# Kernel optimization log

Hardware: AMD Instinct MI355X
Metric: run time of the kernel (lower is better)

## Reference

```python
import jax, jax.numpy as jnp
import numpy as np

D_MODEL = 1024
N_HEADS = 16
DFF = 4096
B, S = 2, 2048
EPS = 1e-6


def _dense_params(key, d_in, d_out):
    kw, kb = jax.random.split(key)
    w = jax.random.normal(kw, (d_in, d_out), jnp.float32) * 0.02
    b = jax.random.normal(kb, (d_out,), jnp.float32) * 0.02
    return w, b


def setup_inputs() -> dict:
    key = jax.random.key(0)
    ks = jax.random.split(key, 20)
    inp = {
        "x": jax.random.normal(ks[0], (B, S, D_MODEL), jnp.float32),
        "enc_output": jax.random.normal(ks[1], (B, S, D_MODEL), jnp.float32),
        # causal look-ahead mask: 1 where attention is NOT allowed
        "look_ahead_mask": jnp.triu(jnp.ones((S, S), jnp.float32), k=1)[None, None],
        "padding_mask": (jax.random.uniform(ks[2], (B, 1, 1, S)) < 0.1).astype(jnp.float32),
    }
    names = ["mha1_wq", "mha1_wk", "mha1_wv", "mha1_wo",
             "mha2_wq", "mha2_wk", "mha2_wv", "mha2_wo"]
    for i, n in enumerate(names):
        w, b = _dense_params(ks[3 + i], D_MODEL, D_MODEL)
        inp[n] = w
        inp[n.replace("w", "b")] = b
    inp["ffn_w1"], inp["ffn_b1"] = _dense_params(ks[11], D_MODEL, DFF)
    inp["ffn_w2"], inp["ffn_b2"] = _dense_params(ks[12], DFF, D_MODEL)
    for i, n in enumerate(["ln1", "ln2", "ln3"]):
        inp[n + "_g"] = jnp.ones((D_MODEL,), jnp.float32)
        inp[n + "_b"] = jnp.zeros((D_MODEL,), jnp.float32)
    return inp


def _layernorm(x, g, b):
    mu = jnp.mean(x, axis=-1, keepdims=True)
    var = jnp.mean(jnp.square(x - mu), axis=-1, keepdims=True)
    return (x - mu) * jax.lax.rsqrt(var + EPS) * g + b


def _mha(v, k, q, mask, wq, bq, wk, bk, wv, bv, wo, bo):
    Bq, Sq, D = q.shape
    depth = D // N_HEADS

    def split(t):  # [B,S,D] -> [B,H,S,depth]
        return t.reshape(t.shape[0], -1, N_HEADS, depth).transpose(0, 2, 1, 3)

    qh = split(q @ wq + bq)
    kh = split(k @ wk + bk)
    vh = split(v @ wv + bv)
    logits = jnp.einsum("bhqd,bhkd->bhqk", qh, kh) / jnp.sqrt(jnp.float32(depth))
    if mask is not None:
        logits = logits + mask * (-1e9)
    attn = jax.nn.softmax(logits, axis=-1)
    out = jnp.einsum("bhqk,bhkd->bhqd", attn, vh)
    out = out.transpose(0, 2, 1, 3).reshape(Bq, Sq, D)
    return out @ wo + bo


def reference(x, enc_output, look_ahead_mask, padding_mask,
              mha1_wq, mha1_bq, mha1_wk, mha1_bk, mha1_wv, mha1_bv, mha1_wo, mha1_bo,
              mha2_wq, mha2_bq, mha2_wk, mha2_bk, mha2_wv, mha2_bv, mha2_wo, mha2_bo,
              ffn_w1, ffn_b1, ffn_w2, ffn_b2,
              ln1_g, ln1_b, ln2_g, ln2_b, ln3_g, ln3_b):
    # self-attention (training=False -> dropout is identity)
    attn1 = _mha(x, x, x, look_ahead_mask,
                 mha1_wq, mha1_bq, mha1_wk, mha1_bk, mha1_wv, mha1_bv, mha1_wo, mha1_bo)
    out1 = _layernorm(x + attn1, ln1_g, ln1_b)
    # cross-attention: q from decoder, k/v from encoder output
    attn2 = _mha(enc_output, enc_output, out1, padding_mask,
                 mha2_wq, mha2_bq, mha2_wk, mha2_bk, mha2_wv, mha2_bv, mha2_wo, mha2_bo)
    out2 = _layernorm(out1 + attn2, ln2_g, ln2_b)
    ffn = jax.nn.relu(out2 @ ffn_w1 + ffn_b1) @ ffn_w2 + ffn_b2
    return _layernorm(out2 + ffn, ln3_g, ln3_b)
```

## Files before the change

kernel.cpp:

```cpp
#include <hip/hip_runtime.h>
#include <hip/hip_bf16.h>
#include <stdint.h>

#define DM   1024
#define NH   16
#define SS   2048
#define BB   2
#define MT   4096

typedef __attribute__((ext_vector_type(8))) short short8;
typedef __attribute__((ext_vector_type(4))) float f32x4;

typedef __attribute__((address_space(1))) const unsigned int as1_uint;
typedef __attribute__((address_space(3))) unsigned int as3_uint;

__device__ __forceinline__ void async16(const void* g, void* l) {
  __builtin_amdgcn_global_load_lds((as1_uint*)g, (as3_uint*)l, 16, 0, 0);
}

#define WAITV(n) asm volatile("s_waitcnt vmcnt(" #n ")" ::: "memory")
#define BARRIER_SB() do { __builtin_amdgcn_s_barrier(); __builtin_amdgcn_sched_barrier(0); } while (0)
#define EXP2(x) __builtin_amdgcn_exp2f(x)

__device__ __forceinline__ unsigned short f2bf(float f) {
  union { float f; unsigned u; } c; c.f = f;
  unsigned r = c.u + 0x7fffu + ((c.u >> 16) & 1u);
  return (unsigned short)(r >> 16);
}

__device__ __forceinline__ unsigned cvt_pk_bf16(float lo, float hi) {
  unsigned r;
  asm("v_cvt_pk_bf16_f32 %0, %1, %2" : "=v"(r) : "v"(lo), "v"(hi));
  return r;
}

__device__ __forceinline__ float swz16(float x) {
  return __uint_as_float((unsigned)__builtin_amdgcn_ds_swizzle((int)__float_as_uint(x), 0x401F));
}

__global__ __launch_bounds__(256) void k_f32_to_bf16(
    const float* __restrict__ in, unsigned short* __restrict__ out, int n) {
  int i = (blockIdx.x * 256 + threadIdx.x) * 4;
  if (i >= n) return;
  float4 v = *(const float4*)(in + i);
  uint2 u;
  u.x = (unsigned)f2bf(v.x) | ((unsigned)f2bf(v.y) << 16);
  u.y = (unsigned)f2bf(v.z) | ((unsigned)f2bf(v.w) << 16);
  *(uint2*)(out + i) = u;
}

__global__ __launch_bounds__(256) void k_transpose_bf16(
    const float* __restrict__ in, unsigned short* __restrict__ out, int R, int C) {
  __shared__ float t[64][65];
  int c0 = blockIdx.x * 64, r0 = blockIdx.y * 64;
  int tx = threadIdx.x & 63, ty = threadIdx.x >> 6;
#pragma unroll
  for (int i = 0; i < 16; i++)
    t[ty + i * 4][tx] = in[(size_t)(r0 + ty + i * 4) * C + c0 + tx];
  __syncthreads();
#pragma unroll
  for (int i = 0; i < 16; i++)
    out[(size_t)(c0 + ty + i * 4) * R + r0 + tx] = f2bf(t[tx][ty + i * 4]);
}

template<int BM, int OUT_MODE, bool RELU, bool RESID, bool SPLITK>
__global__ __launch_bounds__(256) void k_gemm(
    const unsigned short* __restrict__ A,
    const unsigned short* __restrict__ Bt,
    const float* __restrict__ bias,
    const float* __restrict__ resid,
    void* __restrict__ outp, void* __restrict__ outp2,
    int M, int N, int K, int KS) {
  __shared__ unsigned short Alds[3][BM * 32];
  __shared__ unsigned short Blds[3][128 * 32];
  int tid = threadIdx.x;
  int w = tid >> 6, lane = tid & 63;
  int l15 = lane & 15, l4 = lane >> 4;
  int brow = blockIdx.y * BM, bcol = blockIdx.x * 128;

  constexpr int MR = 4;
  constexpr int NR = (BM == 128) ? 4 : 2;
  int wr = (BM == 128) ? (w >> 1) : 0;
  int wc = (BM == 128) ? (w & 1) : w;
  int rbase = wr * 64;
  int cbase = wc * (NR * 16);

  f32x4 acc[MR][NR];
#pragma unroll
  for (int i = 0; i < MR; i++)
#pragma unroll
    for (int j = 0; j < NR; j++) acc[i][j] = (f32x4){0.f, 0.f, 0.f, 0.f};

#define STAGEG(bufi, kk) do {                                                  \
    _Pragma("unroll")                                                          \
    for (int c = 0; c < BM / 64; c++) {                                        \
      int elem = (c * 256 + tid) * 8;                                          \
      int row = elem >> 5, col = elem & 31;                                    \
      async16(A + (size_t)(brow + row) * K + (kk) + col, &Alds[bufi][elem]);   \
    }                                                                          \
    _Pragma("unroll")                                                          \
    for (int c = 0; c < 2; c++) {                                              \
      int elem = (c * 256 + tid) * 8;                                          \
      int row = elem >> 5, col = elem & 31;                                    \
      async16(Bt + (size_t)(bcol + row) * K + (kk) + col, &Blds[bufi][elem]);  \
    } } while (0)

  int kbeg = SPLITK ? blockIdx.z * KS : 0;
  int nk = KS / 32;
  STAGEG(0, kbeg);
  if (nk > 1) {
    STAGEG(1, kbeg + 32);
    if (BM == 128) WAITV(4); else WAITV(3);
  } else {
    WAITV(0);
  }
  BARRIER_SB();

  for (int t = 0; t < nk; t++) {
    int buf = t % 3;
    if (t + 2 < nk) STAGEG((t + 2) % 3, kbeg + (t + 2) * 32);
    short8 af[MR], bfr[NR];
#pragma unroll
    for (int i = 0; i < MR; i++)
      af[i] = *(const short8*)&Alds[buf][(rbase + i * 16 + l15) * 32 + l4 * 8];
#pragma unroll
    for (int j = 0; j < NR; j++)
      bfr[j] = *(const short8*)&Blds[buf][(cbase + j * 16 + l15) * 32 + l4 * 8];
#pragma unroll
    for (int i = 0; i < MR; i++)
#pragma unroll
      for (int j = 0; j < NR; j++)
        acc[i][j] = __builtin_amdgcn_mfma_f32_16x16x32_bf16(af[i], bfr[j], acc[i][j], 0, 0, 0);
    if (t + 2 < nk) {
      if (BM == 128) WAITV(4); else WAITV(3);
    } else if (t + 1 < nk) {
      WAITV(0);
    }
    if (t + 1 < nk) BARRIER_SB();
  }
#undef STAGEG

  void* op = (SPLITK && blockIdx.z) ? outp2 : outp;
#pragma unroll
  for (int i = 0; i < MR; i++)
#pragma unroll
    for (int j = 0; j < NR; j++) {
      int row = brow + rbase + i * 16 + l4 * 4;
      int col = bcol + cbase + j * 16 + l15;
      float bs = (SPLITK || !bias) ? 0.f : bias[col];
#pragma unroll
      for (int r = 0; r < 4; r++) {
        float v = acc[i][j][r] + bs;
        if (RESID) v += resid[(size_t)(row + r) * N + col];
        if (RELU) v = fmaxf(v, 0.f);
        if (OUT_MODE == 0) ((float*)op)[(size_t)(row + r) * N + col] = v;
        else               ((unsigned short*)op)[(size_t)(row + r) * N + col] = f2bf(v);
      }
    }
}

__global__ __launch_bounds__(256) void k_gemm_qkv(
    const unsigned short* __restrict__ a0, const unsigned short* __restrict__ a1,
    const unsigned short* __restrict__ a2,
    const unsigned short* __restrict__ Bt,
    const float* __restrict__ b0, const float* __restrict__ b1, const float* __restrict__ b2,
    unsigned short* __restrict__ o0, unsigned short* __restrict__ o1, unsigned short* __restrict__ o2,
    int vmat, int M, int K) {
  __shared__ unsigned short Alds[3][128 * 32];
  __shared__ unsigned short Blds[3][128 * 32];
  int tid = threadIdx.x;
  int w = tid >> 6, lane = tid & 63;
  int wr = w >> 1, wc = w & 1;
  int l15 = lane & 15, l4 = lane >> 4;
  int z = blockIdx.z;
  const unsigned short* A  = (z == 0) ? a0 : (z == 1) ? a1 : a2;
  const unsigned short* Bz = Bt + (size_t)z * 1048576;
  int brow = blockIdx.y * 128, bcol = blockIdx.x * 128;

  f32x4 acc[4][4];
#pragma unroll
  for (int i = 0; i < 4; i++)
#pragma unroll
    for (int j = 0; j < 4; j++) acc[i][j] = (f32x4){0.f, 0.f, 0.f, 0.f};

#define STAGEQ(bufi, kk) do {                                                  \
    _Pragma("unroll")                                                          \
    for (int c = 0; c < 2; c++) {                                              \
      int elem = (c * 256 + tid) * 8;                                          \
      int row = elem >> 5, col = elem & 31;                                    \
      async16(A + (size_t)(brow + row) * K + (kk) + col, &Alds[bufi][elem]);   \
      async16(Bz + (size_t)(bcol + row) * K + (kk) + col, &Blds[bufi][elem]);  \
    } } while (0)

  int nk = K / 32;
  STAGEQ(0, 0);
  STAGEQ(1, 32);
  WAITV(4);
  BARRIER_SB();

  for (int t = 0; t < nk; t++) {
    int buf = t % 3;
    if (t + 2 < nk) STAGEQ((t + 2) % 3, (t + 2) * 32);
    short8 af[4], bfr[4];
#pragma unroll
    for (int i = 0; i < 4; i++) {
      af[i]  = *(const short8*)&Alds[buf][(wr * 64 + i * 16 + l15) * 32 + l4 * 8];
      bfr[i] = *(const short8*)&Blds[buf][(wc * 64 + i * 16 + l15) * 32 + l4 * 8];
    }
#pragma unroll
    for (int i = 0; i < 4; i++)
#pragma unroll
      for (int j = 0; j < 4; j++)
        acc[i][j] = __builtin_amdgcn_mfma_f32_16x16x32_bf16(af[i], bfr[j], acc[i][j], 0, 0, 0);
    if (t + 2 < nk) WAITV(4);
    else if (t + 1 < nk) WAITV(0);
    if (t + 1 < nk) BARRIER_SB();
  }
#undef STAGEQ

  const float* bias = (z == 0) ? b0 : (z == 1) ? b1 : b2;
  unsigned short* op = (z == 0) ? o0 : (z == 1) ? o1 : o2;
  bool tr = (z == vmat);
#pragma unroll
  for (int i = 0; i < 4; i++)
#pragma unroll
    for (int j = 0; j < 4; j++) {
      int row = brow + wr * 64 + i * 16 + l4 * 4;
      int colL = bcol + wc * 64 + j * 16 + l15;
      float bs = bias[colL];
#pragma unroll
      for (int r = 0; r < 4; r++) {
        float v = acc[i][j][r] + bs;
        if (tr) op[(size_t)colL * M + row + r] = f2bf(v);
        else    op[(size_t)(row + r) * 1024 + colL] = f2bf(v);
      }
    }
}

template<bool CAUSAL>
__global__ __launch_bounds__(256) void k_attn(
    const unsigned short* __restrict__ Q,
    const unsigned short* __restrict__ Kb,
    const unsigned short* __restrict__ Vt,
    const float* __restrict__ pm,
    unsigned short* __restrict__ out) {
  __shared__ unsigned short Klds[3][64 * 64];
  __shared__ unsigned short Vlds[3][64 * 64];
  __shared__ unsigned short Pw[4][2][16 * 72];
  int tid = threadIdx.x, w = tid >> 6, lane = tid & 63;
  int l15 = lane & 15, l4 = lane >> 4;
  int h = blockIdx.y, b = blockIdx.z;
  const float SC = 0.125f * 1.44269504089f;
  const int NPASS = CAUSAL ? 2 : 1;

#define STAGE(bufi, kt_) do {                                                  \
    _Pragma("unroll")                                                          \
    for (int c = 0; c < 2; c++) {                                              \
      int e0 = w * 1024 + c * 512;                                             \
      int elem = e0 + lane * 8;                                                \
      int row_ = elem >> 6;                                                    \
      int col_ = (elem & 63) ^ ((row_ & 7) << 3);                              \
      async16(Kb + (size_t)(b * SS + (kt_) * 64 + row_) * DM + h * 64 + col_,  \
              &Klds[bufi][elem]);                                              \
      async16(Vt + (size_t)(h * 64 + row_) * MT + b * SS + (kt_) * 64 + col_,  \
              &Vlds[bufi][elem]);                                              \
    } } while (0)

  for (int pass = 0; pass < NPASS; pass++) {
    int qt = CAUSAL ? (pass == 0 ? (15 - (int)blockIdx.x) : (int)blockIdx.x)
                    : (int)blockIdx.x;
    int qbase = qt * 128 + w * 32;

    short8 qf[2][2];
#pragma unroll
    for (int f = 0; f < 2; f++) {
      size_t qrow = (size_t)b * SS + qbase + f * 16 + l15;
#pragma unroll
      for (int ks = 0; ks < 2; ks++)
        qf[f][ks] = *(const short8*)(Q + qrow * DM + h * 64 + ks * 32 + l4 * 8);
    }

    float mrow[2] = {-1e30f, -1e30f}, lrow[2] = {0.f, 0.f};
    f32x4 accO[2][4];
#pragma unroll
    for (int f = 0; f < 2; f++)
#pragma unroll
      for (int d = 0; d < 4; d++) accO[f][d] = (f32x4){0.f, 0.f, 0.f, 0.f};

    int ktend = CAUSAL ? (2 * qt + 1) : (SS / 64 - 1);
    if (pass) BARRIER_SB();
    STAGE(0, 0);
    if (ktend >= 1) { STAGE(1, 1); WAITV(4); } else { WAITV(0); }
    BARRIER_SB();

    for (int kt = 0; kt <= ktend; kt++) {
      int buf = kt % 3;
      if (kt + 2 <= ktend) STAGE((kt + 2) % 3, kt + 2);

      bool active = !CAUSAL || (kt * 64 <= qbase + 31);
      if (active) {
        f32x4 sa[2][4];
#pragma unroll
        for (int f = 0; f < 2; f++)
#pragma unroll
          for (int nt = 0; nt < 4; nt++) sa[f][nt] = (f32x4){0.f, 0.f, 0.f, 0.f};
        __builtin_amdgcn_s_setprio(1);
#pragma unroll
        for (int ks = 0; ks < 2; ks++)
#pragma unroll
          for (int nt = 0; nt < 4; nt++) {
            int kr = nt * 16 + l15;
            short8 kf = *(const short8*)&Klds[buf][kr * 64 + ((ks * 32 + l4 * 8) ^ ((kr & 7) << 3))];
#pragma unroll
            for (int f = 0; f < 2; f++)
              sa[f][nt] = __builtin_amdgcn_mfma_f32_16x16x32_bf16(kf, qf[f][ks], sa[f][nt], 0, 0, 0);
          }
        __builtin_amdgcn_s_setprio(0);

        float pmb[16];
        if (!CAUSAL) {
#pragma unroll
          for (int nt = 0; nt < 4; nt++) {
            float4 pmv = *(const float4*)(pm + b * SS + kt * 64 + nt * 16 + l4 * 4);
#pragma unroll
            for (int r = 0; r < 4; r++) pmb[nt * 4 + r] = ((const float*)&pmv)[r] * -1e30f;
          }
        }
        bool diag = CAUSAL && (kt * 64 + 63 > qbase);

        float sv[2][16], tm[2];
#pragma unroll
        for (int f = 0; f < 2; f++) {
          if (CAUSAL && !diag) {
#pragma unroll
            for (int i = 0; i < 16; i++) sv[f][i] = sa[f][i >> 2][i & 3] * SC;
          } else if (CAUSAL) {
#pragma unroll
            for (int nt = 0; nt < 4; nt++)
#pragma unroll
              for (int r = 0; r < 4; r++) {
                float s = sa[f][nt][r] * SC;
                int kg = kt * 64 + nt * 16 + l4 * 4 + r;
                int qg = qbase + f * 16 + l15;
                if (kg > qg) s = -1e30f;
                sv[f][nt * 4 + r] = s;
              }
          } else {
#pragma unroll
            for (int i = 0; i < 16; i++)
              sv[f][i] = fmaf(sa[f][i >> 2][i & 3], SC, pmb[i]);
          }
          float t8[8];
#pragma unroll
          for (int i = 0; i < 8; i++) t8[i] = fmaxf(sv[f][i], sv[f][i + 8]);
#pragma unroll
          for (int i = 0; i < 4; i++) t8[i] = fmaxf(t8[i], t8[i + 4]);
          t8[0] = fmaxf(t8[0], t8[1]);
          t8[2] = fmaxf(t8[2], t8[3]);
          tm[f] = fmaxf(t8[0], t8[2]);
        }

        float sA = swz16(tm[0]);
        float sB = swz16(tm[1]);
        tm[0] = fmaxf(tm[0], sA);
        tm[1] = fmaxf(tm[1], sB);
        float xA = __shfl_xor(tm[0], 32);
        float xB = __shfl_xor(tm[1], 32);
        tm[0] = fmaxf(tm[0], xA);
        tm[1] = fmaxf(tm[1], xB);

#pragma unroll
        for (int f = 0; f < 2; f++) {
          if (!__all(tm[f] - mrow[f] <= 8.f)) {
            float mnew = fmaxf(mrow[f], tm[f]);
            float corr = EXP2(mrow[f] - mnew);
            mrow[f] = mnew;
            lrow[f] *= corr;
#pragma unroll
            for (int r = 0; r < 4; r++) {
              float cq = __shfl(corr, l4 * 4 + r);
#pragma unroll
              for (int dt = 0; dt < 4; dt++) accO[f][dt][r] *= cq;
            }
          }

          float p[16];
#pragma unroll
          for (int i = 0; i < 16; i++) p[i] = EXP2(sv[f][i] - mrow[f]);
          float a8[8];
#pragma unroll
          for (int i = 0; i < 8; i++) a8[i] = p[i] + p[i + 8];
#pragma unroll
          for (int i = 0; i < 4; i++) a8[i] = a8[i] + a8[i + 4];
          lrow[f] += (a8[0] + a8[1]) + (a8[2] + a8[3]);

#pragma unroll
          for (int nt = 0; nt < 4; nt++) {
            uint2 u;
            u.x = cvt_pk_bf16(p[nt * 4 + 0], p[nt * 4 + 1]);
            u.y = cvt_pk_bf16(p[nt * 4 + 2], p[nt * 4 + 3]);
            *(uint2*)&Pw[w][f][l15 * 72 + nt * 16 + l4 * 4] = u;
          }
        }

        __builtin_amdgcn_s_setprio(1);
#pragma unroll
        for (int ks = 0; ks < 2; ks++) {
          short8 pf0 = *(const short8*)&Pw[w][0][l15 * 72 + ks * 32 + l4 * 8];
          short8 pf1 = *(const short8*)&Pw[w][1][l15 * 72 + ks * 32 + l4 * 8];
#pragma unroll
          for (int dt = 0; dt < 4; dt++) {
            int vr = dt * 16 + l15;
            short8 vf = *(const short8*)&Vlds[buf][vr * 64 + ((ks * 32 + l4 * 8) ^ ((vr & 7) << 3))];
            accO[0][dt] = __builtin_amdgcn_mfma_f32_16x16x32_bf16(pf0, vf, accO[0][dt], 0, 0, 0);
            accO[1][dt] = __builtin_amdgcn_mfma_f32_16x16x32_bf16(pf1, vf, accO[1][dt], 0, 0, 0);
          }
        }
        __builtin_amdgcn_s_setprio(0);
      }

      if (kt + 2 <= ktend) WAITV(4);
      else if (kt + 1 <= ktend) WAITV(0);
      if (kt + 1 <= ktend) BARRIER_SB();
    }

#pragma unroll
    for (int f = 0; f < 2; f++) {
      lrow[f] += swz16(lrow[f]);
      lrow[f] += __shfl_xor(lrow[f], 32);
    }
#pragma unroll
    for (int f = 0; f < 2; f++)
#pragma unroll
      for (int r = 0; r < 4; r++) {
        float lq = __shfl(lrow[f], l4 * 4 + r);
        float inv = 1.f / lq;
        size_t row = (size_t)b * SS + qbase + f * 16 + l4 * 4 + r;
#pragma unroll
        for (int dt = 0; dt < 4; dt++)
          out[row * DM + h * 64 + dt * 16 + l15] = f2bf(accO[f][dt][r] * inv);
      }
  }
#undef STAGE
}

__global__ __launch_bounds__(256) void k_ln(
    const float* __restrict__ in, const float* __restrict__ in2,
    const float* __restrict__ resid, const float* __restrict__ bias,
    const float* __restrict__ g, const float* __restrict__ bb,
    float* __restrict__ outf, unsigned short* __restrict__ outb) {
  int row = blockIdx.x, tid = threadIdx.x;
  int w = tid >> 6;
  __shared__ float red[4];
  float4 v = *(const float4*)(in + (size_t)row * 1024 + tid * 4);
  if (in2) {
    float4 v2 = *(const float4*)(in2 + (size_t)row * 1024 + tid * 4);
    v.x += v2.x; v.y += v2.y; v.z += v2.z; v.w += v2.w;
  }
  if (resid) {
    float4 v2 = *(const float4*)(resid + (size_t)row * 1024 + tid * 4);
    v.x += v2.x; v.y += v2.y; v.z += v2.z; v.w += v2.w;
  }
  if (bias) {
    float4 v2 = *(const float4*)(bias + tid * 4);
    v.x += v2.x; v.y += v2.y; v.z += v2.z; v.w += v2.w;
  }
  float s = v.x + v.y + v.z + v.w;
#pragma unroll
  for (int d = 1; d < 64; d <<= 1) s += __shfl_xor(s, d);
  if ((tid & 63) == 0) red[w] = s;
  __syncthreads();
  float mu = (red[0] + red[1] + red[2] + red[3]) * (1.f / 1024.f);
  float d0 = v.x - mu, d1 = v.y - mu, d2 = v.z - mu, d3 = v.w - mu;
  float q = d0 * d0 + d1 * d1 + d2 * d2 + d3 * d3;
#pragma unroll
  for (int d = 1; d < 64; d <<= 1) q += __shfl_xor(q, d);
  __syncthreads();
  if ((tid & 63) == 0) red[w] = q;
  __syncthreads();
  float var = (red[0] + red[1] + red[2] + red[3]) * (1.f / 1024.f);
  float rs = rsqrtf(var + 1e-6f);
  float4 gg = *(const float4*)(g + tid * 4);
  float4 bv = *(const float4*)(bb + tid * 4);
  float y0 = d0 * rs * gg.x + bv.x;
  float y1 = d1 * rs * gg.y + bv.y;
  float y2 = d2 * rs * gg.z + bv.z;
  float y3 = d3 * rs * gg.w + bv.w;
  if (outf) {
    float4 o; o.x = y0; o.y = y1; o.z = y2; o.w = y3;
    *(float4*)(outf + (size_t)row * 1024 + tid * 4) = o;
  }
  if (outb) {
    uint2 u;
    u.x = (unsigned)f2bf(y0) | ((unsigned)f2bf(y1) << 16);
    u.y = (unsigned)f2bf(y2) | ((unsigned)f2bf(y3) << 16);
    *(uint2*)(outb + (size_t)row * 1024 + tid * 4) = u;
  }
}

extern "C" void kernel_launch(void* const* d_in, const int* in_sizes, int n_in,
                              void* d_out, int out_size, void* d_ws, size_t ws_size,
                              hipStream_t stream) {
  const float* x    = (const float*)d_in[0];
  const float* enc  = (const float*)d_in[1];
  const float* pm   = (const float*)d_in[3];
  const float* wq1  = (const float*)d_in[4];   const float* bq1 = (const float*)d_in[5];
  const float* wk1  = (const float*)d_in[6];   const float* bk1 = (const float*)d_in[7];
  const float* wv1  = (const float*)d_in[8];   const float* bv1 = (const float*)d_in[9];
  const float* wo1  = (const float*)d_in[10];  const float* bo1 = (const float*)d_in[11];
  const float* wq2  = (const float*)d_in[12];  const float* bq2 = (const float*)d_in[13];
  const float* wk2  = (const float*)d_in[14];  const float* bk2 = (const float*)d_in[15];
  const float* wv2  = (const float*)d_in[16];  const float* bv2 = (const float*)d_in[17];
  const float* wo2  = (const float*)d_in[18];  const float* bo2 = (const float*)d_in[19];
  const float* fw1  = (const float*)d_in[20];  const float* fb1 = (const float*)d_in[21];
  const float* fw2  = (const float*)d_in[22];  const float* fb2 = (const float*)d_in[23];
  const float* ln1g = (const float*)d_in[24];  const float* ln1b = (const float*)d_in[25];
  const float* ln2g = (const float*)d_in[26];  const float* ln2b = (const float*)d_in[27];
  const float* ln3g = (const float*)d_in[28];  const float* ln3b = (const float*)d_in[29];

  char* ws = (char*)d_ws;
  unsigned short* XB = (unsigned short*)(ws + 0);
  unsigned short* EB = (unsigned short*)(ws + 8388608);
  unsigned short* Qb = (unsigned short*)(ws + 16777216);
  unsigned short* Kb = (unsigned short*)(ws + 25165824);
  unsigned short* Vt = (unsigned short*)(ws + 33554432);
  unsigned short* AT = (unsigned short*)(ws + 41943040);
  float*          T  = (float*)(ws + 50331648);
  float*          R  = (float*)(ws + 67108864);
  unsigned short* RB = (unsigned short*)(ws + 83886080);
  unsigned short* WT0 = (unsigned short*)(ws + 92274688);
  unsigned short* W1T = (unsigned short*)(ws + 92274688 + 16777216);
  unsigned short* W2T = (unsigned short*)(ws + 92274688 + 25165824);
  unsigned short* H   = (unsigned short*)(ws + 0);
  float*          T1  = (float*)(ws + 33554432);
  float*          T1o = (float*)(ws + 16777216);

  k_f32_to_bf16<<<4096, 256, 0, stream>>>(x, XB, MT * DM);
  k_f32_to_bf16<<<4096, 256, 0, stream>>>(enc, EB, MT * DM);
  const float* wlist[8] = {wq1, wk1, wv1, wo1, wq2, wk2, wv2, wo2};
  for (int i = 0; i < 8; i++)
    k_transpose_bf16<<<dim3(16, 16), 256, 0, stream>>>(wlist[i], WT0 + (size_t)i * 1048576, 1024, 1024);
  k_transpose_bf16<<<dim3(64, 16), 256, 0, stream>>>(fw1, W1T, 1024, 4096);
  k_transpose_bf16<<<dim3(16, 64), 256, 0, stream>>>(fw2, W2T, 4096, 1024);

  k_gemm_qkv<<<dim3(8, 32, 3), 256, 0, stream>>>(XB, XB, XB, WT0, bq1, bk1, bv1,
                                                 Qb, Kb, Vt, 2, MT, DM);
  k_attn<true><<<dim3(8, 16, 2), 256, 0, stream>>>(Qb, Kb, Vt, nullptr, AT);
  k_gemm<64, 0, false, false, true><<<dim3(8, 64, 2), 256, 0, stream>>>(
      AT, WT0 + 3 * 1048576, nullptr, nullptr, T, T1o, MT, DM, DM, 512);
  k_ln<<<4096, 256, 0, stream>>>(T, T1o, x, bo1, ln1g, ln1b, R, RB);

  k_gemm_qkv<<<dim3(8, 32, 3), 256, 0, stream>>>(RB, EB, EB, WT0 + 4 * 1048576,
                                                 bq2, bk2, bv2, Qb, Kb, Vt, 2, MT, DM);
  k_attn<false><<<dim3(16, 16, 2), 256, 0, stream>>>(Qb, Kb, Vt, pm, AT);
  k_gemm<64, 0, false, false, true><<<dim3(8, 64, 2), 256, 0, stream>>>(
      AT, WT0 + 7 * 1048576, nullptr, nullptr, T, T1o, MT, DM, DM, 512);
  k_ln<<<4096, 256, 0, stream>>>(T, T1o, R, bo2, ln2g, ln2b, R, RB);

  k_gemm<128, 1, true, false, false><<<dim3(32, 32), 256, 0, stream>>>(
      RB, W1T, fb1, nullptr, H, nullptr, MT, 4096, DM, 1024);
  k_gemm<64, 0, false, false, true><<<dim3(8, 64, 2), 256, 0, stream>>>(
      H, W2T, nullptr, nullptr, T, T1, MT, DM, 4096, 2048);
  k_ln<<<4096, 256, 0, stream>>>(T, T1, R, fb2, ln3g, ln3b, (float*)d_out, nullptr);
}
```

Measured before the change: 465.2 us.

## Load V fragments directly from global into registers instead of LDS staging

Removes the V shared-memory buffers in the attention kernel. Each wave loads its V MFMA operands straight from global memory into registers before the QK^T/softmax phase, overlapping that latency with compute. This reduces LDS footprint and LDS reads and halves the async copies per stage. The trade is that every wave re-reads the same V tile from cache, and register pressure rises, which could hurt occupancy.

```diff
diff --git a/kernel.cpp b/kernel.cpp
--- a/kernel.cpp
+++ b/kernel.cpp
@@ -245,7 +245,6 @@
     const float* __restrict__ pm,
     unsigned short* __restrict__ out) {
   __shared__ unsigned short Klds[3][64 * 64];
-  __shared__ unsigned short Vlds[3][64 * 64];
   __shared__ unsigned short Pw[4][2][16 * 72];
   int tid = threadIdx.x, w = tid >> 6, lane = tid & 63;
   int l15 = lane & 15, l4 = lane >> 4;
@@ -253,7 +252,9 @@
   const float SC = 0.125f * 1.44269504089f;
   const int NPASS = CAUSAL ? 2 : 1;
 
-#define STAGE(bufi, kt_) do {                                                  \
+  const unsigned short* vrow = Vt + (size_t)(h * 64 + l15) * MT + b * SS + l4 * 8;
+
+#define STAGEK(bufi, kt_) do {                                                 \
     _Pragma("unroll")                                                          \
     for (int c = 0; c < 2; c++) {                                              \
       int e0 = w * 1024 + c * 512;                                             \
@@ -262,8 +263,6 @@
       int col_ = (elem & 63) ^ ((row_ & 7) << 3);                              \
       async16(Kb + (size_t)(b * SS + (kt_) * 64 + row_) * DM + h * 64 + col_,  \
               &Klds[bufi][elem]);                                              \
-      async16(Vt + (size_t)(h * 64 + row_) * MT + b * SS + (kt_) * 64 + col_,  \
-              &Vlds[bufi][elem]);                                              \
     } } while (0)
 
   for (int pass = 0; pass < NPASS; pass++) {
@@ -289,15 +288,25 @@
 
     int ktend = CAUSAL ? (2 * qt + 1) : (SS / 64 - 1);
     if (pass) BARRIER_SB();
-    STAGE(0, 0);
-    if (ktend >= 1) { STAGE(1, 1); WAITV(4); } else { WAITV(0); }
+    STAGEK(0, 0);
+    STAGEK(1, 1);
+    WAITV(2);
     BARRIER_SB();
 
     for (int kt = 0; kt <= ktend; kt++) {
       int buf = kt % 3;
-      if (kt + 2 <= ktend) STAGE((kt + 2) % 3, kt + 2);
-
       bool active = !CAUSAL || (kt * 64 <= qbase + 31);
+
+      short8 vreg[2][4];
+      if (active) {
+#pragma unroll
+        for (int ks = 0; ks < 2; ks++)
+#pragma unroll
+          for (int dt = 0; dt < 4; dt++)
+            vreg[ks][dt] = *(const short8*)(vrow + (size_t)(dt * 16) * MT + kt * 64 + ks * 32);
+      }
+      if (kt + 2 <= ktend) STAGEK((kt + 2) % 3, kt + 2);
+
       if (active) {
         f32x4 sa[2][4];
 #pragma unroll
@@ -402,7 +411,12 @@
             *(uint2*)&Pw[w][f][l15 * 72 + nt * 16 + l4 * 4] = u;
           }
         }
-
+      }
+
+      if (kt + 2 <= ktend) WAITV(2);
+      else WAITV(0);
+
+      if (active) {
         __builtin_amdgcn_s_setprio(1);
 #pragma unroll
         for (int ks = 0; ks < 2; ks++) {
@@ -410,17 +424,13 @@
           short8 pf1 = *(const short8*)&Pw[w][1][l15 * 72 + ks * 32 + l4 * 8];
 #pragma unroll
           for (int dt = 0; dt < 4; dt++) {
-            int vr = dt * 16 + l15;
-            short8 vf = *(const short8*)&Vlds[buf][vr * 64 + ((ks * 32 + l4 * 8) ^ ((vr & 7) << 3))];
-            accO[0][dt] = __builtin_amdgcn_mfma_f32_16x16x32_bf16(pf0, vf, accO[0][dt], 0, 0, 0);
-            accO[1][dt] = __builtin_amdgcn_mfma_f32_16x16x32_bf16(pf1, vf, accO[1][dt], 0, 0, 0);
+            accO[0][dt] = __builtin_amdgcn_mfma_f32_16x16x32_bf16(pf0, vreg[ks][dt], accO[0][dt], 0, 0, 0);
+            accO[1][dt] = __builtin_amdgcn_mfma_f32_16x16x32_bf16(pf1, vreg[ks][dt], accO[1][dt], 0, 0, 0);
           }
         }
         __builtin_amdgcn_s_setprio(0);
       }
 
-      if (kt + 2 <= ktend) WAITV(4);
-      else if (kt + 1 <= ktend) WAITV(0);
       if (kt + 1 <= ktend) BARRIER_SB();
     }
 
@@ -441,7 +451,7 @@
           out[row * DM + h * 64 + dt * 16 + l15] = f2bf(accO[f][dt][r] * inv);
       }
   }
-#undef STAGE
+#undef STAGEK
 }
 
 __global__ __launch_bounds__(256) void k_ln(
```

Result: slower. 519.6 us (+11.7%).
